# Kernel optimization log

Measured on AMD Instinct MI355X. Metric: run time of the kernel, lower is better.

The kernel has to match this reference:

```python
import jax, jax.numpy as jnp
import numpy as np

N_A, N_B = 100000, 50000
F_IN, C = 32, 64
L, G = 2, 4  # conv layers per gate, gates (i,f,o,c)
E_AA, E_AB, E_BB = 1600000, 800000, 800000


def setup_inputs() -> dict:
    key = jax.random.key(0)
    ks = jax.random.split(key, 15)
    return {
        "x_a": jax.random.normal(ks[0], (N_A, F_IN), jnp.float32),
        "x_b": jax.random.normal(ks[1], (N_B, F_IN), jnp.float32),
        "c_a": jax.random.normal(ks[2], (N_A, C), jnp.float32),
        "c_b": jax.random.normal(ks[3], (N_B, C), jnp.float32),
        "lin_w": jax.random.normal(ks[4], (G, 2, F_IN, C), jnp.float32) * 0.1,
        "lin_b": jax.random.uniform(ks[5], (G, 2, C), jnp.float32),
        "conv_wl": jax.random.normal(ks[6], (G, L, 3, C, C), jnp.float32) * 0.1,
        "conv_wr": jax.random.normal(ks[7], (G, L, 3, C, C), jnp.float32) * 0.1,
        "conv_b": jax.random.uniform(ks[8], (G, L, 3, C), jnp.float32) * 0.1,
        "src_aa": jax.random.randint(ks[9], (E_AA,), 0, N_A),
        "dst_aa": jax.random.randint(ks[10], (E_AA,), 0, N_A),
        "src_ab": jax.random.randint(ks[11], (E_AB,), 0, N_A),
        "dst_ab": jax.random.randint(ks[12], (E_AB,), 0, N_B),
        "src_bb": jax.random.randint(ks[13], (E_BB,), 0, N_B),
        "dst_bb": jax.random.randint(ks[14], (E_BB,), 0, N_B),
    }


def _seg_mean(x_src, src, dst, n_dst):
    # SAGEConv mean aggregation; empty destinations get 0 (PyG semantics)
    s = jax.ops.segment_sum(x_src[src], dst, num_segments=n_dst)
    cnt = jax.ops.segment_sum(jnp.ones((src.shape[0], 1), x_src.dtype), dst, num_segments=n_dst)
    return s / jnp.maximum(cnt, 1.0)


def _gate(g, x_a, x_b, lin_w, lin_b, conv_wl, conv_wr, conv_b, idx):
    src_aa, dst_aa, src_ab, dst_ab, src_bb, dst_bb = idx
    t_a = x_a @ lin_w[g, 0]
    t_b = x_b @ lin_w[g, 1]
    for l in range(L):
        # edge type 0: a->a (dst a)
        agg_aa = _seg_mean(t_a, src_aa, dst_aa, N_A)
        na = agg_aa @ conv_wl[g, l, 0] + t_a @ conv_wr[g, l, 0] + conv_b[g, l, 0]
        # edge types 1: a->b and 2: b->b, HeteroConv sums both into dst b
        agg_ab = _seg_mean(t_a, src_ab, dst_ab, N_B)
        agg_bb = _seg_mean(t_b, src_bb, dst_bb, N_B)
        nb = (agg_ab @ conv_wl[g, l, 1] + t_b @ conv_wr[g, l, 1] + conv_b[g, l, 1]
              + agg_bb @ conv_wl[g, l, 2] + t_b @ conv_wr[g, l, 2] + conv_b[g, l, 2])
        t_a, t_b = na, nb
    return lin_b[g, 0] + t_a, lin_b[g, 1] + t_b


def reference(x_a, x_b, c_a, c_b, lin_w, lin_b, conv_wl, conv_wr, conv_b,
              src_aa, dst_aa, src_ab, dst_ab, src_bb, dst_bb):
    idx = (src_aa, dst_aa, src_ab, dst_ab, src_bb, dst_bb)
    i_a, i_b = map(jax.nn.sigmoid, _gate(0, x_a, x_b, lin_w, lin_b, conv_wl, conv_wr, conv_b, idx))
    f_a, f_b = map(jax.nn.sigmoid, _gate(1, x_a, x_b, lin_w, lin_b, conv_wl, conv_wr, conv_b, idx))
    o_a, o_b = map(jax.nn.sigmoid, _gate(2, x_a, x_b, lin_w, lin_b, conv_wl, conv_wr, conv_b, idx))
    g_a, g_b = map(jnp.tanh, _gate(3, x_a, x_b, lin_w, lin_b, conv_wl, conv_wr, conv_b, idx))
    cn_a = f_a * c_a + i_a * g_a
    cn_b = f_b * c_b + i_b * g_b
    h_a = o_a * jnp.tanh(cn_a)
    h_b = o_b * jnp.tanh(cn_b)
    return (h_a, h_b, cn_a, cn_b)
```

## Files before the change

kernel.cpp:

```cpp
#include <hip/hip_runtime.h>
#include <hip/hip_bf16.h>

#define NA 100000
#define NB 50000
#define EAA 1600000
#define EAB 800000
#define EBB 800000

#define NBKAA 782
#define NBKB  391
#define BKA 200
#define BKB 100
#define DCAP 4096

#define GFA 1563
#define GFB 782

typedef __hip_bfloat16 bf16;
typedef __attribute__((ext_vector_type(8))) short bf16x8;
typedef __attribute__((ext_vector_type(4))) float f32x4;

__device__ __forceinline__ float u2f(unsigned short u) {
  union { unsigned int i; float f; } x; x.i = ((unsigned int)u) << 16; return x.f;
}
__device__ __forceinline__ unsigned short f2u(float f) {
  __hip_bfloat16 h = __float2bfloat16(f);
  return *reinterpret_cast<unsigned short*>(&h);
}
__device__ __forceinline__ short f2bs(float f) {
  __hip_bfloat16 h = __float2bfloat16(f);
  return *reinterpret_cast<short*>(&h);
}
__device__ __forceinline__ float fast_sigmoid(float z) {
  return 1.f / (1.f + __expf(-z));
}
__device__ __forceinline__ float fast_tanh(float z) {
  z = fminf(fmaxf(z, -15.f), 15.f);
  float t = __expf(2.f * z);
  return (t - 1.f) / (t + 1.f);
}

__global__ __launch_bounds__(256) void kA_bin(
    const int* __restrict__ d1, const int* __restrict__ d2, const int* __restrict__ d3,
    int* __restrict__ binAA, int* __restrict__ binAB, int* __restrict__ binBB) {
  __shared__ int h[1024];
  int blk = blockIdx.x;
  const int* dst; int* out; int e0, nbk;
  if (blk < BKA)            { dst = d1; out = binAA + blk * NBKAA; e0 = blk * 8000; nbk = NBKAA; }
  else if (blk < BKA + BKB) { int k = blk - BKA; dst = d2; out = binAB + k * NBKB; e0 = k * 8000; nbk = NBKB; }
  else                      { int k = blk - BKA - BKB; dst = d3; out = binBB + k * NBKB; e0 = k * 8000; nbk = NBKB; }
  for (int i = threadIdx.x; i < nbk; i += 256) h[i] = 0;
  __syncthreads();
  for (int i = threadIdx.x; i < 8000; i += 256) atomicAdd(&h[dst[e0 + i] >> 7], 1);
  __syncthreads();
  for (int i = threadIdx.x; i < nbk; i += 256) out[i] = h[i];
}

__global__ __launch_bounds__(256) void kB1(
    int* __restrict__ binAA, int* __restrict__ binAB, int* __restrict__ binBB,
    int* __restrict__ totAA, int* __restrict__ totAB, int* __restrict__ totBB) {
  int wave = threadIdx.x >> 6, lane = threadIdx.x & 63;
  int wid = blockIdx.x * 4 + wave;
  int* bin; int* tot; int b, nblk, nbk;
  if (wid < NBKAA)              { bin = binAA; tot = totAA; b = wid; nblk = BKA; nbk = NBKAA; }
  else if (wid < NBKAA + NBKB)  { bin = binAB; tot = totAB; b = wid - NBKAA; nblk = BKB; nbk = NBKB; }
  else                          { bin = binBB; tot = totBB; b = wid - NBKAA - NBKB; nblk = BKB; nbk = NBKB; }
  int C = (nblk + 63) / 64;
  int vals[4]; int s = 0;
  for (int j = 0; j < C; ++j) { int k = lane * C + j; vals[j] = (k < nblk) ? bin[k * nbk + b] : 0; s += vals[j]; }
  int pre = s;
  for (int o = 1; o < 64; o <<= 1) { int x = __shfl_up(pre, o); if (lane >= o) pre += x; }
  int run = pre - s;
  for (int j = 0; j < C; ++j) { int k = lane * C + j; if (k < nblk) { int v = vals[j]; bin[k * nbk + b] = run; run += v; } }
  if (lane == 63) tot[b] = pre;
}

__global__ __launch_bounds__(256) void kB2(
    const int* __restrict__ totAA, const int* __restrict__ totAB, const int* __restrict__ totBB,
    int* __restrict__ bsAA, int* __restrict__ bsAB, int* __restrict__ bsBB) {
  __shared__ int part[256];
  int set = blockIdx.x; const int* tot; int* bs; int nbk;
  if (set == 0)      { tot = totAA; bs = bsAA; nbk = NBKAA; }
  else if (set == 1) { tot = totAB; bs = bsAB; nbk = NBKB; }
  else               { tot = totBB; bs = bsBB; nbk = NBKB; }
  int t = threadIdx.x;
  int v[4]; int s = 0;
  #pragma unroll
  for (int j = 0; j < 4; ++j) { int k = t * 4 + j; v[j] = (k < nbk) ? tot[k] : 0; s += v[j]; }
  part[t] = s;
  __syncthreads();
  for (int o = 1; o < 256; o <<= 1) {
    int x = (t >= o) ? part[t - o] : 0;
    __syncthreads();
    part[t] += x;
    __syncthreads();
  }
  int run = part[t] - s;
  #pragma unroll
  for (int j = 0; j < 4; ++j) { int k = t * 4 + j; if (k < nbk) { bs[k] = run; run += v[j]; } }
  if (t == 255) bs[nbk] = part[255];
}

__global__ __launch_bounds__(256) void kC_scatter(
    const int* __restrict__ s1, const int* __restrict__ d1,
    const int* __restrict__ s2, const int* __restrict__ d2,
    const int* __restrict__ s3, const int* __restrict__ d3,
    const int* __restrict__ binAA, const int* __restrict__ binAB, const int* __restrict__ binBB,
    const int* __restrict__ bsAA, const int* __restrict__ bsAB, const int* __restrict__ bsBB,
    int* __restrict__ pkAA, int* __restrict__ pkAB, int* __restrict__ pkBB) {
  __shared__ int baseL[1024];
  __shared__ int run[1024];
  int blk = blockIdx.x;
  const int* src; const int* dst; const int* bin; const int* bs; int* pk; int e0, nbk, bofs;
  if (blk < BKA)            { src = s1; dst = d1; bin = binAA; bs = bsAA; pk = pkAA; e0 = blk * 8000; nbk = NBKAA; bofs = blk * NBKAA; }
  else if (blk < BKA + BKB) { int k = blk - BKA; src = s2; dst = d2; bin = binAB; bs = bsAB; pk = pkAB; e0 = k * 8000; nbk = NBKB; bofs = k * NBKB; }
  else                      { int k = blk - BKA - BKB; src = s3; dst = d3; bin = binBB; bs = bsBB; pk = pkBB; e0 = k * 8000; nbk = NBKB; bofs = k * NBKB; }
  for (int i = threadIdx.x; i < nbk; i += 256) { baseL[i] = bs[i] + bin[bofs + i]; run[i] = 0; }
  __syncthreads();
  for (int i = threadIdx.x; i < 8000; i += 256) {
    int d = dst[e0 + i];
    int b = d >> 7;
    int off = atomicAdd(&run[b], 1);
    pk[baseL[b] + off] = src[e0 + i] | ((d & 127) << 24);
  }
}

__global__ __launch_bounds__(256) void kD_nodesort(
    const int* __restrict__ pkAA, const int* __restrict__ pkAB, const int* __restrict__ pkBB,
    const int* __restrict__ bsAA, const int* __restrict__ bsAB, const int* __restrict__ bsBB,
    int* __restrict__ colAA, int* __restrict__ colAB, int* __restrict__ colBB,
    int* __restrict__ stAA, int* __restrict__ ctAA,
    int* __restrict__ stAB, int* __restrict__ ctAB,
    int* __restrict__ stBB, int* __restrict__ ctBB) {
  __shared__ int hist[128], nodeOff[129], run[128];
  __shared__ int stage[DCAP];
  int wid = blockIdx.x;
  const int* pk; const int* bs; int* col; int* stn; int* ctn; int b, N;
  if (wid < NBKAA)             { pk = pkAA; bs = bsAA; col = colAA; stn = stAA; ctn = ctAA; b = wid; N = NA; }
  else if (wid < NBKAA + NBKB) { pk = pkAB; bs = bsAB; col = colAB; stn = stAB; ctn = ctAB; b = wid - NBKAA; N = NB; }
  else                         { pk = pkBB; bs = bsBB; col = colBB; stn = stBB; ctn = ctBB; b = wid - NBKAA - NBKB; N = NB; }
  int node0 = b * 128;
  int base = bs[b], cntB = bs[b + 1] - base;
  int t = threadIdx.x;
  if (t < 128) hist[t] = 0;
  __syncthreads();
  for (int i = t; i < cntB; i += 256) atomicAdd(&hist[pk[base + i] >> 24], 1);
  __syncthreads();
  if (t < 64) {
    int v0 = hist[2 * t], v1 = hist[2 * t + 1];
    int s = v0 + v1; int pre = s;
    for (int o = 1; o < 64; o <<= 1) { int x = __shfl_up(pre, o); if (t >= o) pre += x; }
    int ex = pre - s;
    nodeOff[2 * t] = ex; nodeOff[2 * t + 1] = ex + v0;
    if (t == 63) nodeOff[128] = pre;
    run[2 * t] = 0; run[2 * t + 1] = 0;
  }
  __syncthreads();
  if (t < 128) {
    int n = node0 + t;
    if (n < N) { ctn[n] = hist[t]; stn[n] = base + nodeOff[t]; }
  }
  if (cntB <= DCAP) {
    for (int i = t; i < cntB; i += 256) {
      int e = pk[base + i]; int ln = e >> 24;
      int off = atomicAdd(&run[ln], 1);
      stage[nodeOff[ln] + off] = e & 0xFFFFFF;
    }
    __syncthreads();
    for (int i = t; i < cntB; i += 256) col[base + i] = stage[i];
  } else {
    for (int i = t; i < cntB; i += 256) {
      int e = pk[base + i]; int ln = e >> 24;
      int off = atomicAdd(&run[ln], 1);
      col[base + nodeOff[ln] + off] = e & 0xFFFFFF;
    }
  }
}

__global__ __launch_bounds__(256) void k_cast2(const float* __restrict__ xa, const float* __restrict__ xb,
                                               bf16* __restrict__ ya, bf16* __restrict__ yb) {
  int i = blockIdx.x * 256 + threadIdx.x;
  const float* x; bf16* y; int base;
  if (i < 800000)       { x = xa; y = ya; base = i * 4; }
  else if (i < 1200000) { x = xb; y = yb; base = (i - 800000) * 4; }
  else return;
  float4 v = *(const float4*)(x + base);
  ushort4 o; o.x = f2u(v.x); o.y = f2u(v.y); o.z = f2u(v.z); o.w = f2u(v.w);
  *(ushort4*)(y + base) = o;
}

__global__ __launch_bounds__(256) void kW1(
    const float* __restrict__ lin_w, const float* __restrict__ wl, const float* __restrict__ wr,
    float* __restrict__ Mbuf) {
  __shared__ float Ls[32][64];
  __shared__ float Rs[64][64];
  int id = blockIdx.x, term = id >> 2, g = id & 3;
  const float* L = lin_w + ((size_t)g * 2 + (term >= 3 ? 1 : 0)) * 2048;
  const float* R1; const float* R2 = nullptr;
  switch (term) {
    case 0: R1 = wl + ((size_t)(g * 2) * 3 + 0) * 4096; break;
    case 1: R1 = wr + ((size_t)(g * 2) * 3 + 0) * 4096; break;
    case 2: R1 = wl + ((size_t)(g * 2) * 3 + 1) * 4096; break;
    case 3: R1 = wl + ((size_t)(g * 2) * 3 + 2) * 4096; break;
    default: R1 = wr + ((size_t)(g * 2) * 3 + 1) * 4096; R2 = wr + ((size_t)(g * 2) * 3 + 2) * 4096; break;
  }
  for (int i = threadIdx.x; i < 2048; i += 256) Ls[i >> 6][i & 63] = L[i];
  for (int i = threadIdx.x; i < 4096; i += 256) Rs[i >> 6][i & 63] = R2 ? (R1[i] + R2[i]) : R1[i];
  __syncthreads();
  int c = threadIdx.x & 63, rq = threadIdx.x >> 6;
  float acc[8] = {0, 0, 0, 0, 0, 0, 0, 0};
  for (int k = 0; k < 64; ++k) {
    float rv = Rs[k][c];
    #pragma unroll
    for (int i = 0; i < 8; ++i) acc[i] += Ls[rq * 8 + i][k] * rv;
  }
  #pragma unroll
  for (int i = 0; i < 8; ++i)
    Mbuf[(size_t)(term * 4 + g) * 2048 + (rq * 8 + i) * 64 + c] = acc[i];
}

__global__ __launch_bounds__(256) void kW2(
    const float* __restrict__ Mbuf, const float* __restrict__ wl, const float* __restrict__ wr,
    const float* __restrict__ cbv, const float* __restrict__ lin_b,
    bf16* __restrict__ Wfrag, float* __restrict__ Bv) {
  __shared__ float Ps[2][32][65];
  __shared__ float Ws[2][64][64];
  int blk = blockIdx.x;
  if (blk >= 36) {
    int g = blk - 36;
    if (threadIdx.x < 64) {
      int c = threadIdx.x;
      const float* b00 = cbv + (size_t)((g * 2 + 0) * 3 + 0) * 64;
      const float* b10 = cbv + (size_t)((g * 2 + 0) * 3 + 1) * 64;
      const float* b20 = cbv + (size_t)((g * 2 + 0) * 3 + 2) * 64;
      const float* b01 = cbv + (size_t)((g * 2 + 1) * 3 + 0) * 64;
      const float* b11 = cbv + (size_t)((g * 2 + 1) * 3 + 1) * 64;
      const float* b21 = cbv + (size_t)((g * 2 + 1) * 3 + 2) * 64;
      const float* wl01 = wl + (size_t)((g * 2 + 1) * 3 + 0) * 4096;
      const float* wl11 = wl + (size_t)((g * 2 + 1) * 3 + 1) * 4096;
      const float* wl21 = wl + (size_t)((g * 2 + 1) * 3 + 2) * 4096;
      const float* wr01 = wr + (size_t)((g * 2 + 1) * 3 + 0) * 4096;
      const float* wr11 = wr + (size_t)((g * 2 + 1) * 3 + 1) * 4096;
      const float* wr21 = wr + (size_t)((g * 2 + 1) * 3 + 2) * 4096;
      float s_maa = 0.f, s_ca = 0.f, s_mab = 0.f, s_mbb = 0.f, s_cb = 0.f;
      for (int k = 0; k < 64; ++k) {
        float v0 = b00[k], vb = b10[k] + b20[k];
        s_maa += v0 * wl01[k * 64 + c];
        s_ca  += v0 * wr01[k * 64 + c];
        s_mab += v0 * wl11[k * 64 + c];
        s_mbb += vb * wl21[k * 64 + c];
        s_cb  += vb * (wr11[k * 64 + c] + wr21[k * 64 + c]);
      }
      Bv[(g * 5 + 0) * 64 + c] = s_maa;
      Bv[(g * 5 + 1) * 64 + c] = s_ca + b01[c] + lin_b[(g * 2 + 0) * 64 + c];
      Bv[(g * 5 + 2) * 64 + c] = s_mab;
      Bv[(g * 5 + 3) * 64 + c] = s_mbb;
      Bv[(g * 5 + 4) * 64 + c] = s_cb + b11[c] + b21[c] + lin_b[(g * 2 + 1) * 64 + c];
    }
    return;
  }
  int mat = blk, g, m;
  if (blk < 12) { g = blk / 3; m = blk % 3; }
  else          { g = (blk - 12) / 6; m = (blk - 12) % 6 + 3; }
  const float* wl01 = wl + (size_t)((g * 2 + 1) * 3 + 0) * 4096;
  const float* wl11 = wl + (size_t)((g * 2 + 1) * 3 + 1) * 4096;
  const float* wl21 = wl + (size_t)((g * 2 + 1) * 3 + 2) * 4096;
  const float* wr01 = wr + (size_t)((g * 2 + 1) * 3 + 0) * 4096;
  const float* wr11 = wr + (size_t)((g * 2 + 1) * 3 + 1) * 4096;
  const float* wr21 = wr + (size_t)((g * 2 + 1) * 3 + 2) * 4096;
  int   p1t, p2t = -1;
  const float *w1a = nullptr, *w1b = nullptr, *w2a = nullptr, *w2b = nullptr;
  switch (m) {
    case 0: p1t = 0; w1a = wl01; break;
    case 1: p1t = 1; w1a = wl01; p2t = 0; w2a = wr01; break;
    case 2: p1t = 1; w1a = wr01; break;
    case 3: p1t = 0; w1a = wl11; break;
    case 4: p1t = 1; w1a = wl11; p2t = 2; w2a = wr11; w2b = wr21; break;
    case 5: p1t = 2; w1a = wl21; break;
    case 6: p1t = 3; w1a = wl21; break;
    case 7: p1t = 3; w1a = wr11; w1b = wr21; p2t = 4; w2a = wl21; break;
    default: p1t = 4; w1a = wr11; w1b = wr21; break;
  }
  int nprod = (p2t >= 0) ? 2 : 1;
  for (int i = threadIdx.x; i < 2048; i += 256) Ps[0][i >> 6][i & 63] = Mbuf[(size_t)(p1t * 4 + g) * 2048 + i];
  for (int i = threadIdx.x; i < 4096; i += 256) Ws[0][i >> 6][i & 63] = w1b ? (w1a[i] + w1b[i]) : w1a[i];
  if (nprod == 2) {
    for (int i = threadIdx.x; i < 2048; i += 256) Ps[1][i >> 6][i & 63] = Mbuf[(size_t)(p2t * 4 + g) * 2048 + i];
    for (int i = threadIdx.x; i < 4096; i += 256) Ws[1][i >> 6][i & 63] = w2b ? (w2a[i] + w2b[i]) : w2a[i];
  }
  __syncthreads();
  int nt = threadIdx.x >> 6, lane = threadIdx.x & 63;
  int c = nt * 16 + (lane & 15), kb = (lane >> 4) * 8;
  float acc[8] = {0, 0, 0, 0, 0, 0, 0, 0};
  for (int k = 0; k < 64; ++k) {
    float w1v = Ws[0][k][c];
    #pragma unroll
    for (int j = 0; j < 8; ++j) acc[j] += Ps[0][kb + j][k] * w1v;
  }
  if (nprod == 2) {
    for (int k = 0; k < 64; ++k) {
      float w2v = Ws[1][k][c];
      #pragma unroll
      for (int j = 0; j < 8; ++j) acc[j] += Ps[1][kb + j][k] * w2v;
    }
  }
  bf16x8 v;
  #pragma unroll
  for (int j = 0; j < 8; ++j) v[j] = f2bs(acc[j]);
  *(bf16x8*)(Wfrag + ((size_t)(mat * 4 + nt) * 64 + lane) * 8) = v;
}

__global__ __launch_bounds__(256) void k_aggP1(
    const bf16* __restrict__ xa, const bf16* __restrict__ xb,
    bf16* __restrict__ P, bf16* __restrict__ Q, bf16* __restrict__ R,
    const int* __restrict__ st_aa, const int* __restrict__ ct_aa, const int* __restrict__ col_aa,
    const int* __restrict__ st_ab, const int* __restrict__ ct_ab, const int* __restrict__ col_ab,
    const int* __restrict__ st_bb, const int* __restrict__ ct_bb, const int* __restrict__ col_bb) {
  int b = blockIdx.x;
  const bf16* src; bf16* dst; const int* start; const int* cnt; const int* col; int n0;
  if (b < 25000)      { src = xa; dst = P; start = st_aa; cnt = ct_aa; col = col_aa; n0 = b * 4; }
  else if (b < 37500) { src = xa; dst = Q; start = st_ab; cnt = ct_ab; col = col_ab; n0 = (b - 25000) * 4; }
  else                { src = xb; dst = R; start = st_bb; cnt = ct_bb; col = col_bb; n0 = (b - 37500) * 4; }
  int wave = threadIdx.x >> 6, lane = threadIdx.x & 63;
  int n = n0 + wave;
  int e8 = lane >> 3, c8 = lane & 7;
  int st = start[n];
  int deg = cnt[n];
  float s0 = 0.f, s1 = 0.f, s2 = 0.f, s3 = 0.f;
  #pragma unroll 2
  for (int e = e8; e < deg; e += 8) {
    int i = col[st + e];
    ushort4 v = *(const ushort4*)(src + (size_t)i * 32 + c8 * 4);
    s0 += u2f(v.x); s1 += u2f(v.y); s2 += u2f(v.z); s3 += u2f(v.w);
  }
  s0 += __shfl_xor(s0, 8);  s1 += __shfl_xor(s1, 8);  s2 += __shfl_xor(s2, 8);  s3 += __shfl_xor(s3, 8);
  s0 += __shfl_xor(s0, 16); s1 += __shfl_xor(s1, 16); s2 += __shfl_xor(s2, 16); s3 += __shfl_xor(s3, 16);
  s0 += __shfl_xor(s0, 32); s1 += __shfl_xor(s1, 32); s2 += __shfl_xor(s2, 32); s3 += __shfl_xor(s3, 32);
  if (e8 == 0) {
    float inv = 1.f / (float)(deg > 1 ? deg : 1);
    ushort4 o; o.x = f2u(s0 * inv); o.y = f2u(s1 * inv); o.z = f2u(s2 * inv); o.w = f2u(s3 * inv);
    *(ushort4*)(dst + (size_t)n * 32 + c8 * 4) = o;
  }
}

__global__ __launch_bounds__(256) void k_aggP2(
    const bf16* __restrict__ P, const bf16* __restrict__ Q, const bf16* __restrict__ R,
    bf16* __restrict__ P2, bf16* __restrict__ Q2, bf16* __restrict__ S, bf16* __restrict__ T,
    const int* __restrict__ st_aa, const int* __restrict__ ct_aa, const int* __restrict__ col_aa,
    const int* __restrict__ st_ab, const int* __restrict__ ct_ab, const int* __restrict__ col_ab,
    const int* __restrict__ st_bb, const int* __restrict__ ct_bb, const int* __restrict__ col_bb) {
  int b = blockIdx.x;
  int wave = threadIdx.x >> 6, lane = threadIdx.x & 63;
  int e8 = lane >> 3, c8 = lane & 7;
  if (b < 37500) {
    const bf16* src; bf16* dst; const int* start; const int* cnt; const int* col; int n0;
    if (b < 25000) { src = P; dst = P2; start = st_aa; cnt = ct_aa; col = col_aa; n0 = b * 4; }
    else           { src = P; dst = Q2; start = st_ab; cnt = ct_ab; col = col_ab; n0 = (b - 25000) * 4; }
    int n = n0 + wave;
    int st = start[n];
    int deg = cnt[n];
    float s0 = 0.f, s1 = 0.f, s2 = 0.f, s3 = 0.f;
    #pragma unroll 2
    for (int e = e8; e < deg; e += 8) {
      int i = col[st + e];
      ushort4 v = *(const ushort4*)(src + (size_t)i * 32 + c8 * 4);
      s0 += u2f(v.x); s1 += u2f(v.y); s2 += u2f(v.z); s3 += u2f(v.w);
    }
    s0 += __shfl_xor(s0, 8);  s1 += __shfl_xor(s1, 8);  s2 += __shfl_xor(s2, 8);  s3 += __shfl_xor(s3, 8);
    s0 += __shfl_xor(s0, 16); s1 += __shfl_xor(s1, 16); s2 += __shfl_xor(s2, 16); s3 += __shfl_xor(s3, 16);
    s0 += __shfl_xor(s0, 32); s1 += __shfl_xor(s1, 32); s2 += __shfl_xor(s2, 32); s3 += __shfl_xor(s3, 32);
    if (e8 == 0) {
      float inv = 1.f / (float)(deg > 1 ? deg : 1);
      ushort4 o; o.x = f2u(s0 * inv); o.y = f2u(s1 * inv); o.z = f2u(s2 * inv); o.w = f2u(s3 * inv);
      *(ushort4*)(dst + (size_t)n * 32 + c8 * 4) = o;
    }
  } else {
    int n = (b - 37500) * 4 + wave;
    int st = st_bb[n];
    int deg = ct_bb[n];
    float q0 = 0.f, q1 = 0.f, q2 = 0.f, q3 = 0.f;
    float r0 = 0.f, r1 = 0.f, r2 = 0.f, r3 = 0.f;
    for (int e = e8; e < deg; e += 8) {
      int i = col_bb[st + e];
      ushort4 vq = *(const ushort4*)(Q + (size_t)i * 32 + c8 * 4);
      ushort4 vr = *(const ushort4*)(R + (size_t)i * 32 + c8 * 4);
      q0 += u2f(vq.x); q1 += u2f(vq.y); q2 += u2f(vq.z); q3 += u2f(vq.w);
      r0 += u2f(vr.x); r1 += u2f(vr.y); r2 += u2f(vr.z); r3 += u2f(vr.w);
    }
    q0 += __shfl_xor(q0, 8);  q1 += __shfl_xor(q1, 8);  q2 += __shfl_xor(q2, 8);  q3 += __shfl_xor(q3, 8);
    r0 += __shfl_xor(r0, 8);  r1 += __shfl_xor(r1, 8);  r2 += __shfl_xor(r2, 8);  r3 += __shfl_xor(r3, 8);
    q0 += __shfl_xor(q0, 16); q1 += __shfl_xor(q1, 16); q2 += __shfl_xor(q2, 16); q3 += __shfl_xor(q3, 16);
    r0 += __shfl_xor(r0, 16); r1 += __shfl_xor(r1, 16); r2 += __shfl_xor(r2, 16); r3 += __shfl_xor(r3, 16);
    q0 += __shfl_xor(q0, 32); q1 += __shfl_xor(q1, 32); q2 += __shfl_xor(q2, 32); q3 += __shfl_xor(q3, 32);
    r0 += __shfl_xor(r0, 32); r1 += __shfl_xor(r1, 32); r2 += __shfl_xor(r2, 32); r3 += __shfl_xor(r3, 32);
    if (e8 == 0) {
      float inv = 1.f / (float)(deg > 1 ? deg : 1);
      ushort4 o1v; o1v.x = f2u(q0 * inv); o1v.y = f2u(q1 * inv); o1v.z = f2u(q2 * inv); o1v.w = f2u(q3 * inv);
      *(ushort4*)(S + (size_t)n * 32 + c8 * 4) = o1v;
      ushort4 o2v; o2v.x = f2u(r0 * inv); o2v.y = f2u(r1 * inv); o2v.z = f2u(r2 * inv); o2v.w = f2u(r3 * inv);
      *(ushort4*)(T + (size_t)n * 32 + c8 * 4) = o2v;
    }
  }
}

__global__ __launch_bounds__(256, 2) void k_fin(
    const bf16* __restrict__ xa, const bf16* __restrict__ P, const bf16* __restrict__ P2,
    const bf16* __restrict__ xb, const bf16* __restrict__ Q, const bf16* __restrict__ R,
    const bf16* __restrict__ Q2, const bf16* __restrict__ S, const bf16* __restrict__ T,
    const bf16* __restrict__ Wfrag, const float* __restrict__ Bv,
    const int* __restrict__ cnt_aa, const int* __restrict__ cnt_ab, const int* __restrict__ cnt_bb,
    const float* __restrict__ c_a, const float* __restrict__ c_b,
    float* __restrict__ out) {
  int blk = blockIdx.x;
  int wave = threadIdx.x >> 6, lane = threadIdx.x & 63;
  int l15 = lane & 15, l4 = lane >> 4;
  const size_t TOTA = (size_t)NA * 64, TOTB = (size_t)NB * 64;
  #define FRAG(mat, nt) (*(const bf16x8*)(Wfrag + ((size_t)((mat) * 4 + (nt)) * 64 + lane) * 8))

  if (blk < GFA) {
    int row0 = (blk * 4 + wave) * 16;
    int r = row0 + l15;
    bool ok = r < NA;
    bf16x8 a0 = {0,0,0,0,0,0,0,0}, a1 = a0, a2 = a0;
    if (ok) {
      a0 = *(const bf16x8*)(P2 + (size_t)r * 32 + l4 * 8);
      a1 = *(const bf16x8*)(P  + (size_t)r * 32 + l4 * 8);
      a2 = *(const bf16x8*)(xa + (size_t)r * 32 + l4 * 8);
    }
    f32x4 z[4][4];
    #pragma unroll
    for (int g = 0; g < 4; ++g) {
      #pragma unroll
      for (int nt = 0; nt < 4; ++nt) {
        f32x4 acc = {0.f, 0.f, 0.f, 0.f};
        acc = __builtin_amdgcn_mfma_f32_16x16x32_bf16(a0, FRAG(g * 3 + 0, nt), acc, 0, 0, 0);
        acc = __builtin_amdgcn_mfma_f32_16x16x32_bf16(a1, FRAG(g * 3 + 1, nt), acc, 0, 0, 0);
        acc = __builtin_amdgcn_mfma_f32_16x16x32_bf16(a2, FRAG(g * 3 + 2, nt), acc, 0, 0, 0);
        z[g][nt] = acc;
      }
    }
    float m[4];
    #pragma unroll
    for (int q = 0; q < 4; ++q) {
      int rr = row0 + l4 * 4 + q;
      m[q] = (rr < NA && cnt_aa[rr] > 0) ? 1.f : 0.f;
    }
    float* h = out;
    float* cn = out + TOTA + TOTB;
    #pragma unroll
    for (int nt = 0; nt < 4; ++nt) {
      int col = nt * 16 + l15;
      #pragma unroll
      for (int q = 0; q < 4; ++q) {
        int rr = row0 + l4 * 4 + q;
        if (rr >= NA) continue;
        float zi = z[0][nt][q] + m[q] * Bv[(0 * 5 + 0) * 64 + col] + Bv[(0 * 5 + 1) * 64 + col];
        float zf = z[1][nt][q] + m[q] * Bv[(1 * 5 + 0) * 64 + col] + Bv[(1 * 5 + 1) * 64 + col];
        float zo = z[2][nt][q] + m[q] * Bv[(2 * 5 + 0) * 64 + col] + Bv[(2 * 5 + 1) * 64 + col];
        float zg = z[3][nt][q] + m[q] * Bv[(3 * 5 + 0) * 64 + col] + Bv[(3 * 5 + 1) * 64 + col];
        float ig = fast_sigmoid(zi);
        float fg = fast_sigmoid(zf);
        float og = fast_sigmoid(zo);
        float gg = fast_tanh(zg);
        size_t idx = (size_t)rr * 64 + col;
        float cv = fg * c_a[idx] + ig * gg;
        h[idx] = og * fast_tanh(cv);
        cn[idx] = cv;
      }
    }
  } else {
    int bb = blk - GFA;
    int row0 = (bb * 4 + wave) * 16;
    int r = row0 + l15;
    bool ok = r < NB;
    bf16x8 a0 = {0,0,0,0,0,0,0,0}, a1 = a0, a2 = a0, a3 = a0, a4 = a0, a5 = a0;
    if (ok) {
      a0 = *(const bf16x8*)(Q2 + (size_t)r * 32 + l4 * 8);
      a1 = *(const bf16x8*)(Q  + (size_t)r * 32 + l4 * 8);
      a2 = *(const bf16x8*)(S  + (size_t)r * 32 + l4 * 8);
      a3 = *(const bf16x8*)(T  + (size_t)r * 32 + l4 * 8);
      a4 = *(const bf16x8*)(R  + (size_t)r * 32 + l4 * 8);
      a5 = *(const bf16x8*)(xb + (size_t)r * 32 + l4 * 8);
    }
    f32x4 z[4][4];
    #pragma unroll
    for (int g = 0; g < 4; ++g) {
      #pragma unroll
      for (int nt = 0; nt < 4; ++nt) {
        int mb = 12 + g * 6;
        f32x4 acc = {0.f, 0.f, 0.f, 0.f};
        acc = __builtin_amdgcn_mfma_f32_16x16x32_bf16(a0, FRAG(mb + 0, nt), acc, 0, 0, 0);
        acc = __builtin_amdgcn_mfma_f32_16x16x32_bf16(a1, FRAG(mb + 1, nt), acc, 0, 0, 0);
        acc = __builtin_amdgcn_mfma_f32_16x16x32_bf16(a2, FRAG(mb + 2, nt), acc, 0, 0, 0);
        acc = __builtin_amdgcn_mfma_f32_16x16x32_bf16(a3, FRAG(mb + 3, nt), acc, 0, 0, 0);
        acc = __builtin_amdgcn_mfma_f32_16x16x32_bf16(a4, FRAG(mb + 4, nt), acc, 0, 0, 0);
        acc = __builtin_amdgcn_mfma_f32_16x16x32_bf16(a5, FRAG(mb + 5, nt), acc, 0, 0, 0);
        z[g][nt] = acc;
      }
    }
    float mab[4], mbb[4];
    #pragma unroll
    for (int q = 0; q < 4; ++q) {
      int rr = row0 + l4 * 4 + q;
      bool okr = rr < NB;
      mab[q] = (okr && cnt_ab[rr] > 0) ? 1.f : 0.f;
      mbb[q] = (okr && cnt_bb[rr] > 0) ? 1.f : 0.f;
    }
    float* h = out + TOTA;
    float* cn = out + 2 * TOTA + TOTB;
    #pragma unroll
    for (int nt = 0; nt < 4; ++nt) {
      int col = nt * 16 + l15;
      #pragma unroll
      for (int q = 0; q < 4; ++q) {
        int rr = row0 + l4 * 4 + q;
        if (rr >= NB) continue;
        float zi = z[0][nt][q] + mab[q] * Bv[(0 * 5 + 2) * 64 + col] + mbb[q] * Bv[(0 * 5 + 3) * 64 + col] + Bv[(0 * 5 + 4) * 64 + col];
        float zf = z[1][nt][q] + mab[q] * Bv[(1 * 5 + 2) * 64 + col] + mbb[q] * Bv[(1 * 5 + 3) * 64 + col] + Bv[(1 * 5 + 4) * 64 + col];
        float zo = z[2][nt][q] + mab[q] * Bv[(2 * 5 + 2) * 64 + col] + mbb[q] * Bv[(2 * 5 + 3) * 64 + col] + Bv[(2 * 5 + 4) * 64 + col];
        float zg = z[3][nt][q] + mab[q] * Bv[(3 * 5 + 2) * 64 + col] + mbb[q] * Bv[(3 * 5 + 3) * 64 + col] + Bv[(3 * 5 + 4) * 64 + col];
        float ig = fast_sigmoid(zi);
        float fg = fast_sigmoid(zf);
        float og = fast_sigmoid(zo);
        float gg = fast_tanh(zg);
        size_t idx = (size_t)rr * 64 + col;
        float cv = fg * c_b[idx] + ig * gg;
        h[idx] = og * fast_tanh(cv);
        cn[idx] = cv;
      }
    }
  }
  #undef FRAG
}

extern "C" void kernel_launch(void* const* d_in, const int* in_sizes, int n_in,
                              void* d_out, int out_size, void* d_ws, size_t ws_size,
                              hipStream_t stream) {
  (void)in_sizes; (void)n_in; (void)out_size; (void)ws_size;
  const float* x_a    = (const float*)d_in[0];
  const float* x_b    = (const float*)d_in[1];
  const float* c_a    = (const float*)d_in[2];
  const float* c_b    = (const float*)d_in[3];
  const float* lin_w  = (const float*)d_in[4];
  const float* lin_b  = (const float*)d_in[5];
  const float* conv_wl = (const float*)d_in[6];
  const float* conv_wr = (const float*)d_in[7];
  const float* conv_cb = (const float*)d_in[8];
  const int* src_aa = (const int*)d_in[9];
  const int* dst_aa = (const int*)d_in[10];
  const int* src_ab = (const int*)d_in[11];
  const int* dst_ab = (const int*)d_in[12];
  const int* src_bb = (const int*)d_in[13];
  const int* dst_bb = (const int*)d_in[14];

  char* ws = (char*)d_ws;
  size_t off = 0;
  auto alloc = [&](size_t bytes) -> char* {
    off = (off + 255) & ~(size_t)255;
    char* p = ws + off;
    off += bytes;
    return p;
  };
  bf16* xab = (bf16*)alloc((size_t)NA * 32 * 2);
  bf16* xbb = (bf16*)alloc((size_t)NB * 32 * 2);
  bf16* P   = (bf16*)alloc((size_t)NA * 32 * 2);
  bf16* P2  = (bf16*)alloc((size_t)NA * 32 * 2);
  bf16* Q   = (bf16*)alloc((size_t)NB * 32 * 2);
  bf16* R   = (bf16*)alloc((size_t)NB * 32 * 2);
  bf16* Q2  = (bf16*)alloc((size_t)NB * 32 * 2);
  bf16* S   = (bf16*)alloc((size_t)NB * 32 * 2);
  bf16* T   = (bf16*)alloc((size_t)NB * 32 * 2);
  float* Mbuf = (float*)alloc((size_t)20 * 2048 * 4);
  bf16* Wfrag = (bf16*)alloc((size_t)36 * 4 * 64 * 8 * 2);
  float* Bv = (float*)alloc((size_t)4 * 5 * 64 * 4);
  int* col_aa  = (int*)alloc((size_t)EAA * 4);
  int* col_ab  = (int*)alloc((size_t)EAB * 4);
  int* col_bb  = (int*)alloc((size_t)EBB * 4);
  int* pk_aa   = (int*)alloc((size_t)EAA * 4);
  int* pk_ab   = (int*)alloc((size_t)EAB * 4);
  int* pk_bb   = (int*)alloc((size_t)EBB * 4);
  int* start_aa = (int*)alloc((size_t)NA * 4);
  int* start_ab = (int*)alloc((size_t)NB * 4);
  int* start_bb = (int*)alloc((size_t)NB * 4);
  int* cnt_aa  = (int*)alloc((size_t)NA * 4);
  int* cnt_ab  = (int*)alloc((size_t)NB * 4);
  int* cnt_bb  = (int*)alloc((size_t)NB * 4);
  int* binAA   = (int*)alloc((size_t)BKA * NBKAA * 4);
  int* binAB   = (int*)alloc((size_t)BKB * NBKB * 4);
  int* binBB   = (int*)alloc((size_t)BKB * NBKB * 4);
  int* totAA   = (int*)alloc((size_t)NBKAA * 4);
  int* totAB   = (int*)alloc((size_t)NBKB * 4);
  int* totBB   = (int*)alloc((size_t)NBKB * 4);
  int* bsAA    = (int*)alloc((size_t)(NBKAA + 1) * 4);
  int* bsAB    = (int*)alloc((size_t)(NBKB + 1) * 4);
  int* bsBB    = (int*)alloc((size_t)(NBKB + 1) * 4);

  kW1<<<20, 256, 0, stream>>>(lin_w, conv_wl, conv_wr, Mbuf);
  kW2<<<40, 256, 0, stream>>>(Mbuf, conv_wl, conv_wr, conv_cb, lin_b, Wfrag, Bv);
  k_cast2<<<4688, 256, 0, stream>>>(x_a, x_b, xab, xbb);

  kA_bin<<<BKA + 2 * BKB, 256, 0, stream>>>(dst_aa, dst_ab, dst_bb, binAA, binAB, binBB);
  kB1<<<(NBKAA + 2 * NBKB) / 4, 256, 0, stream>>>(binAA, binAB, binBB, totAA, totAB, totBB);
  kB2<<<3, 256, 0, stream>>>(totAA, totAB, totBB, bsAA, bsAB, bsBB);
  kC_scatter<<<BKA + 2 * BKB, 256, 0, stream>>>(src_aa, dst_aa, src_ab, dst_ab, src_bb, dst_bb,
                                                binAA, binAB, binBB, bsAA, bsAB, bsBB,
                                                pk_aa, pk_ab, pk_bb);
  kD_nodesort<<<NBKAA + 2 * NBKB, 256, 0, stream>>>(pk_aa, pk_ab, pk_bb, bsAA, bsAB, bsBB,
                                                    col_aa, col_ab, col_bb,
                                                    start_aa, cnt_aa, start_ab, cnt_ab,
                                                    start_bb, cnt_bb);

  k_aggP1<<<50000, 256, 0, stream>>>(xab, xbb, P, Q, R,
                                     start_aa, cnt_aa, col_aa,
                                     start_ab, cnt_ab, col_ab,
                                     start_bb, cnt_bb, col_bb);
  k_aggP2<<<50000, 256, 0, stream>>>(P, Q, R, P2, Q2, S, T,
                                     start_aa, cnt_aa, col_aa,
                                     start_ab, cnt_ab, col_ab,
                                     start_bb, cnt_bb, col_bb);

  k_fin<<<GFA + GFB, 256, 0, stream>>>(xab, P, P2, xbb, Q, R, Q2, S, T,
                                       Wfrag, Bv, cnt_aa, cnt_ab, cnt_bb,
                                       c_a, c_b, (float*)d_out);
}
```

Before: 304.2 us.

## Shrink edge blocks, widen gather loads, and process 32 rows per wave in k_fin

Result: slower. 334.3 us (+9.9%).

```diff
diff --git a/kernel.cpp b/kernel.cpp
--- a/kernel.cpp
+++ b/kernel.cpp
@@ -9,12 +9,13 @@
 
 #define NBKAA 782
 #define NBKB  391
-#define BKA 200
-#define BKB 100
+#define EPB 2000
+#define BKA 800
+#define BKB 400
 #define DCAP 4096
 
-#define GFA 1563
-#define GFB 782
+#define GF2A 782
+#define GF2B 391
 
 typedef __hip_bfloat16 bf16;
 typedef __attribute__((ext_vector_type(8))) short bf16x8;
@@ -46,12 +47,12 @@
   __shared__ int h[1024];
   int blk = blockIdx.x;
   const int* dst; int* out; int e0, nbk;
-  if (blk < BKA)            { dst = d1; out = binAA + blk * NBKAA; e0 = blk * 8000; nbk = NBKAA; }
-  else if (blk < BKA + BKB) { int k = blk - BKA; dst = d2; out = binAB + k * NBKB; e0 = k * 8000; nbk = NBKB; }
-  else                      { int k = blk - BKA - BKB; dst = d3; out = binBB + k * NBKB; e0 = k * 8000; nbk = NBKB; }
+  if (blk < BKA)            { dst = d1; out = binAA + blk * NBKAA; e0 = blk * EPB; nbk = NBKAA; }
+  else if (blk < BKA + BKB) { int k = blk - BKA; dst = d2; out = binAB + k * NBKB; e0 = k * EPB; nbk = NBKB; }
+  else                      { int k = blk - BKA - BKB; dst = d3; out = binBB + k * NBKB; e0 = k * EPB; nbk = NBKB; }
   for (int i = threadIdx.x; i < nbk; i += 256) h[i] = 0;
   __syncthreads();
-  for (int i = threadIdx.x; i < 8000; i += 256) atomicAdd(&h[dst[e0 + i] >> 7], 1);
+  for (int i = threadIdx.x; i < EPB; i += 256) atomicAdd(&h[dst[e0 + i] >> 7], 1);
   __syncthreads();
   for (int i = threadIdx.x; i < nbk; i += 256) out[i] = h[i];
 }
@@ -66,7 +67,7 @@
   else if (wid < NBKAA + NBKB)  { bin = binAB; tot = totAB; b = wid - NBKAA; nblk = BKB; nbk = NBKB; }
   else                          { bin = binBB; tot = totBB; b = wid - NBKAA - NBKB; nblk = BKB; nbk = NBKB; }
   int C = (nblk + 63) / 64;
-  int vals[4]; int s = 0;
+  int vals[16]; int s = 0;
   for (int j = 0; j < C; ++j) { int k = lane * C + j; vals[j] = (k < nblk) ? bin[k * nbk + b] : 0; s += vals[j]; }
   int pre = s;
   for (int o = 1; o < 64; o <<= 1) { int x = __shfl_up(pre, o); if (lane >= o) pre += x; }
@@ -112,12 +113,12 @@
   __shared__ int run[1024];
   int blk = blockIdx.x;
   const int* src; const int* dst; const int* bin; const int* bs; int* pk; int e0, nbk, bofs;
-  if (blk < BKA)            { src = s1; dst = d1; bin = binAA; bs = bsAA; pk = pkAA; e0 = blk * 8000; nbk = NBKAA; bofs = blk * NBKAA; }
-  else if (blk < BKA + BKB) { int k = blk - BKA; src = s2; dst = d2; bin = binAB; bs = bsAB; pk = pkAB; e0 = k * 8000; nbk = NBKB; bofs = k * NBKB; }
-  else                      { int k = blk - BKA - BKB; src = s3; dst = d3; bin = binBB; bs = bsBB; pk = pkBB; e0 = k * 8000; nbk = NBKB; bofs = k * NBKB; }
+  if (blk < BKA)            { src = s1; dst = d1; bin = binAA; bs = bsAA; pk = pkAA; e0 = blk * EPB; nbk = NBKAA; bofs = blk * NBKAA; }
+  else if (blk < BKA + BKB) { int k = blk - BKA; src = s2; dst = d2; bin = binAB; bs = bsAB; pk = pkAB; e0 = k * EPB; nbk = NBKB; bofs = k * NBKB; }
+  else                      { int k = blk - BKA - BKB; src = s3; dst = d3; bin = binBB; bs = bsBB; pk = pkBB; e0 = k * EPB; nbk = NBKB; bofs = k * NBKB; }
   for (int i = threadIdx.x; i < nbk; i += 256) { baseL[i] = bs[i] + bin[bofs + i]; run[i] = 0; }
   __syncthreads();
-  for (int i = threadIdx.x; i < 8000; i += 256) {
+  for (int i = threadIdx.x; i < EPB; i += 256) {
     int d = dst[e0 + i];
     int b = d >> 7;
     int off = atomicAdd(&run[b], 1);
@@ -310,6 +311,30 @@
   *(bf16x8*)(Wfrag + ((size_t)(mat * 4 + nt) * 64 + lane) * 8) = v;
 }
 
+__device__ __forceinline__ void acc8(float* s, uint4 v) {
+  s[0] += u2f((unsigned short)(v.x & 0xFFFF)); s[1] += u2f((unsigned short)(v.x >> 16));
+  s[2] += u2f((unsigned short)(v.y & 0xFFFF)); s[3] += u2f((unsigned short)(v.y >> 16));
+  s[4] += u2f((unsigned short)(v.z & 0xFFFF)); s[5] += u2f((unsigned short)(v.z >> 16));
+  s[6] += u2f((unsigned short)(v.w & 0xFFFF)); s[7] += u2f((unsigned short)(v.w >> 16));
+}
+__device__ __forceinline__ void red16(float* s) {
+  #pragma unroll
+  for (int j = 0; j < 8; ++j) {
+    s[j] += __shfl_xor(s[j], 4);
+    s[j] += __shfl_xor(s[j], 8);
+    s[j] += __shfl_xor(s[j], 16);
+    s[j] += __shfl_xor(s[j], 32);
+  }
+}
+__device__ __forceinline__ uint4 pack8(const float* s, float inv) {
+  uint4 o;
+  o.x = (unsigned)f2u(s[0] * inv) | ((unsigned)f2u(s[1] * inv) << 16);
+  o.y = (unsigned)f2u(s[2] * inv) | ((unsigned)f2u(s[3] * inv) << 16);
+  o.z = (unsigned)f2u(s[4] * inv) | ((unsigned)f2u(s[5] * inv) << 16);
+  o.w = (unsigned)f2u(s[6] * inv) | ((unsigned)f2u(s[7] * inv) << 16);
+  return o;
+}
+
 __global__ __launch_bounds__(256) void k_aggP1(
     const bf16* __restrict__ xa, const bf16* __restrict__ xb,
     bf16* __restrict__ P, bf16* __restrict__ Q, bf16* __restrict__ R,
@@ -323,23 +348,19 @@
   else                { src = xb; dst = R; start = st_bb; cnt = ct_bb; col = col_bb; n0 = (b - 37500) * 4; }
   int wave = threadIdx.x >> 6, lane = threadIdx.x & 63;
   int n = n0 + wave;
-  int e8 = lane >> 3, c8 = lane & 7;
+  int e16 = lane >> 2, c4 = lane & 3;
   int st = start[n];
   int deg = cnt[n];
-  float s0 = 0.f, s1 = 0.f, s2 = 0.f, s3 = 0.f;
-  #pragma unroll 2
-  for (int e = e8; e < deg; e += 8) {
+  float s[8] = {0, 0, 0, 0, 0, 0, 0, 0};
+  for (int e = e16; e < deg; e += 16) {
     int i = col[st + e];
-    ushort4 v = *(const ushort4*)(src + (size_t)i * 32 + c8 * 4);
-    s0 += u2f(v.x); s1 += u2f(v.y); s2 += u2f(v.z); s3 += u2f(v.w);
-  }
-  s0 += __shfl_xor(s0, 8);  s1 += __shfl_xor(s1, 8);  s2 += __shfl_xor(s2, 8);  s3 += __shfl_xor(s3, 8);
-  s0 += __shfl_xor(s0, 16); s1 += __shfl_xor(s1, 16); s2 += __shfl_xor(s2, 16); s3 += __shfl_xor(s3, 16);
-  s0 += __shfl_xor(s0, 32); s1 += __shfl_xor(s1, 32); s2 += __shfl_xor(s2, 32); s3 += __shfl_xor(s3, 32);
-  if (e8 == 0) {
+    uint4 v = *(const uint4*)(src + (size_t)i * 32 + c4 * 8);
+    acc8(s, v);
+  }
+  red16(s);
+  if (e16 == 0) {
     float inv = 1.f / (float)(deg > 1 ? deg : 1);
-    ushort4 o; o.x = f2u(s0 * inv); o.y = f2u(s1 * inv); o.z = f2u(s2 * inv); o.w = f2u(s3 * inv);
-    *(ushort4*)(dst + (size_t)n * 32 + c8 * 4) = o;
+    *(uint4*)(dst + (size_t)n * 32 + c4 * 8) = pack8(s, inv);
   }
 }
 
@@ -351,7 +372,7 @@
     const int* __restrict__ st_bb, const int* __restrict__ ct_bb, const int* __restrict__ col_bb) {
   int b = blockIdx.x;
   int wave = threadIdx.x >> 6, lane = threadIdx.x & 63;
-  int e8 = lane >> 3, c8 = lane & 7;
+  int e16 = lane >> 2, c4 = lane & 3;
   if (b < 37500) {
     const bf16* src; bf16* dst; const int* start; const int* cnt; const int* col; int n0;
     if (b < 25000) { src = P; dst = P2; start = st_aa; cnt = ct_aa; col = col_aa; n0 = b * 4; }
@@ -359,51 +380,41 @@
     int n = n0 + wave;
     int st = start[n];
     int deg = cnt[n];
-    float s0 = 0.f, s1 = 0.f, s2 = 0.f, s3 = 0.f;
-    #pragma unroll 2
-    for (int e = e8; e < deg; e += 8) {
+    float s[8] = {0, 0, 0, 0, 0, 0, 0, 0};
+    for (int e = e16; e < deg; e += 16) {
       int i = col[st + e];
-      ushort4 v = *(const ushort4*)(src + (size_t)i * 32 + c8 * 4);
-      s0 += u2f(v.x); s1 += u2f(v.y); s2 += u2f(v.z); s3 += u2f(v.w);
-    }
-    s0 += __shfl_xor(s0, 8);  s1 += __shfl_xor(s1, 8);  s2 += __shfl_xor(s2, 8);  s3 += __shfl_xor(s3, 8);
-    s0 += __shfl_xor(s0, 16); s1 += __shfl_xor(s1, 16); s2 += __shfl_xor(s2, 16); s3 += __shfl_xor(s3, 16);
-    s0 += __shfl_xor(s0, 32); s1 += __shfl_xor(s1, 32); s2 += __shfl_xor(s2, 32); s3 += __shfl_xor(s3, 32);
-    if (e8 == 0) {
+      uint4 v = *(const uint4*)(src + (size_t)i * 32 + c4 * 8);
+      acc8(s, v);
+    }
+    red16(s);
+    if (e16 == 0) {
       float inv = 1.f / (float)(deg > 1 ? deg : 1);
-      ushort4 o; o.x = f2u(s0 * inv); o.y = f2u(s1 * inv); o.z = f2u(s2 * inv); o.w = f2u(s3 * inv);
-      *(ushort4*)(dst + (size_t)n * 32 + c8 * 4) = o;
+      *(uint4*)(dst + (size_t)n * 32 + c4 * 8) = pack8(s, inv);
     }
   } else {
     int n = (b - 37500) * 4 + wave;
     int st = st_bb[n];
     int deg = ct_bb[n];
-    float q0 = 0.f, q1 = 0.f, q2 = 0.f, q3 = 0.f;
-    float r0 = 0.f, r1 = 0.f, r2 = 0.f, r3 = 0.f;
-    for (int e = e8; e < deg; e += 8) {
+    float sq[8] = {0, 0, 0, 0, 0, 0, 0, 0};
+    float sr[8] = {0, 0, 0, 0, 0, 0, 0, 0};
+    for (int e = e16; e < deg; e += 16) {
       int i = col_bb[st + e];
-      ushort4 vq = *(const ushort4*)(Q + (size_t)i * 32 + c8 * 4);
-      ushort4 vr = *(const ushort4*)(R + (size_t)i * 32 + c8 * 4);
-      q0 += u2f(vq.x); q1 += u2f(vq.y); q2 += u2f(vq.z); q3 += u2f(vq.w);
-      r0 += u2f(vr.x); r1 += u2f(vr.y); r2 += u2f(vr.z); r3 += u2f(vr.w);
-    }
-    q0 += __shfl_xor(q0, 8);  q1 += __shfl_xor(q1, 8);  q2 += __shfl_xor(q2, 8);  q3 += __shfl_xor(q3, 8);
-    r0 += __shfl_xor(r0, 8);  r1 += __shfl_xor(r1, 8);  r2 += __shfl_xor(r2, 8);  r3 += __shfl_xor(r3, 8);
-    q0 += __shfl_xor(q0, 16); q1 += __shfl_xor(q1, 16); q2 += __shfl_xor(q2, 16); q3 += __shfl_xor(q3, 16);
-    r0 += __shfl_xor(r0, 16); r1 += __shfl_xor(r1, 16); r2 += __shfl_xor(r2, 16); r3 += __shfl_xor(r3, 16);
-    q0 += __shfl_xor(q0, 32); q1 += __shfl_xor(q1, 32); q2 += __shfl_xor(q2, 32); q3 += __shfl_xor(q3, 32);
-    r0 += __shfl_xor(r0, 32); r1 += __shfl_xor(r1, 32); r2 += __shfl_xor(r2, 32); r3 += __shfl_xor(r3, 32);
-    if (e8 == 0) {
+      uint4 vq = *(const uint4*)(Q + (size_t)i * 32 + c4 * 8);
+      uint4 vr = *(const uint4*)(R + (size_t)i * 32 + c4 * 8);
+      acc8(sq, vq);
+      acc8(sr, vr);
+    }
+    red16(sq);
+    red16(sr);
+    if (e16 == 0) {
       float inv = 1.f / (float)(deg > 1 ? deg : 1);
-      ushort4 o1v; o1v.x = f2u(q0 * inv); o1v.y = f2u(q1 * inv); o1v.z = f2u(q2 * inv); o1v.w = f2u(q3 * inv);
-      *(ushort4*)(S + (size_t)n * 32 + c8 * 4) = o1v;
-      ushort4 o2v; o2v.x = f2u(r0 * inv); o2v.y = f2u(r1 * inv); o2v.z = f2u(r2 * inv); o2v.w = f2u(r3 * inv);
-      *(ushort4*)(T + (size_t)n * 32 + c8 * 4) = o2v;
-    }
-  }
-}
-
-__global__ __launch_bounds__(256, 2) void k_fin(
+      *(uint4*)(S + (size_t)n * 32 + c4 * 8) = pack8(sq, inv);
+      *(uint4*)(T + (size_t)n * 32 + c4 * 8) = pack8(sr, inv);
+    }
+  }
+}
+
+__global__ __launch_bounds__(256) void k_fin(
     const bf16* __restrict__ xa, const bf16* __restrict__ P, const bf16* __restrict__ P2,
     const bf16* __restrict__ xb, const bf16* __restrict__ Q, const bf16* __restrict__ R,
     const bf16* __restrict__ Q2, const bf16* __restrict__ S, const bf16* __restrict__ T,
@@ -416,117 +427,151 @@
   int l15 = lane & 15, l4 = lane >> 4;
   const size_t TOTA = (size_t)NA * 64, TOTB = (size_t)NB * 64;
   #define FRAG(mat, nt) (*(const bf16x8*)(Wfrag + ((size_t)((mat) * 4 + (nt)) * 64 + lane) * 8))
-
-  if (blk < GFA) {
-    int row0 = (blk * 4 + wave) * 16;
-    int r = row0 + l15;
-    bool ok = r < NA;
-    bf16x8 a0 = {0,0,0,0,0,0,0,0}, a1 = a0, a2 = a0;
-    if (ok) {
-      a0 = *(const bf16x8*)(P2 + (size_t)r * 32 + l4 * 8);
-      a1 = *(const bf16x8*)(P  + (size_t)r * 32 + l4 * 8);
-      a2 = *(const bf16x8*)(xa + (size_t)r * 32 + l4 * 8);
-    }
-    f32x4 z[4][4];
+  const bf16x8 z8 = {0, 0, 0, 0, 0, 0, 0, 0};
+
+  if (blk < GF2A) {
+    int row0 = (blk * 4 + wave) * 32;
+    bf16x8 a[3][2];
+    float m[2][4];
     #pragma unroll
-    for (int g = 0; g < 4; ++g) {
-      #pragma unroll
-      for (int nt = 0; nt < 4; ++nt) {
-        f32x4 acc = {0.f, 0.f, 0.f, 0.f};
-        acc = __builtin_amdgcn_mfma_f32_16x16x32_bf16(a0, FRAG(g * 3 + 0, nt), acc, 0, 0, 0);
-        acc = __builtin_amdgcn_mfma_f32_16x16x32_bf16(a1, FRAG(g * 3 + 1, nt), acc, 0, 0, 0);
-        acc = __builtin_amdgcn_mfma_f32_16x16x32_bf16(a2, FRAG(g * 3 + 2, nt), acc, 0, 0, 0);
-        z[g][nt] = acc;
+    for (int s = 0; s < 2; ++s) {
+      int r = row0 + s * 16 + l15;
+      bool ok = r < NA;
+      a[0][s] = ok ? *(const bf16x8*)(P2 + (size_t)r * 32 + l4 * 8) : z8;
+      a[1][s] = ok ? *(const bf16x8*)(P  + (size_t)r * 32 + l4 * 8) : z8;
+      a[2][s] = ok ? *(const bf16x8*)(xa + (size_t)r * 32 + l4 * 8) : z8;
+      #pragma unroll
+      for (int q = 0; q < 4; ++q) {
+        int rr = row0 + s * 16 + l4 * 4 + q;
+        m[s][q] = (rr < NA && cnt_aa[rr] > 0) ? 1.f : 0.f;
       }
-    }
-    float m[4];
-    #pragma unroll
-    for (int q = 0; q < 4; ++q) {
-      int rr = row0 + l4 * 4 + q;
-      m[q] = (rr < NA && cnt_aa[rr] > 0) ? 1.f : 0.f;
     }
     float* h = out;
     float* cn = out + TOTA + TOTB;
     #pragma unroll
     for (int nt = 0; nt < 4; ++nt) {
       int col = nt * 16 + l15;
+      bf16x8 fr[12];
+      #pragma unroll
+      for (int gq = 0; gq < 12; ++gq) fr[gq] = FRAG(gq, nt);
+      float bm[4], bc[4];
+      #pragma unroll
+      for (int g = 0; g < 4; ++g) { bm[g] = Bv[(g * 5 + 0) * 64 + col]; bc[g] = Bv[(g * 5 + 1) * 64 + col]; }
+      #pragma unroll
+      for (int s = 0; s < 2; ++s) {
+        float cpre[4];
+        #pragma unroll
+        for (int q = 0; q < 4; ++q) {
+          int rr = row0 + s * 16 + l4 * 4 + q;
+          cpre[q] = (rr < NA) ? c_a[(size_t)rr * 64 + col] : 0.f;
+        }
+        f32x4 z[4];
+        #pragma unroll
+        for (int g = 0; g < 4; ++g) {
+          f32x4 acc = {0.f, 0.f, 0.f, 0.f};
+          acc = __builtin_amdgcn_mfma_f32_16x16x32_bf16(a[0][s], fr[g * 3 + 0], acc, 0, 0, 0);
+          acc = __builtin_amdgcn_mfma_f32_16x16x32_bf16(a[1][s], fr[g * 3 + 1], acc, 0, 0, 0);
+          acc = __builtin_amdgcn_mfma_f32_16x16x32_bf16(a[2][s], fr[g * 3 + 2], acc, 0, 0, 0);
+          z[g] = acc;
+        }
+        #pragma unroll
+        for (int q = 0; q < 4; ++q) {
+          int rr = row0 + s * 16 + l4 * 4 + q;
+          if (rr >= NA) continue;
+          float zi = z[0][q] + m[s][q] * bm[0] + bc[0];
+          float zf = z[1][q] + m[s][q] * bm[1] + bc[1];
+          float zo = z[2][q] + m[s][q] * bm[2] + bc[2];
+          float zg = z[3][q] + m[s][q] * bm[3] + bc[3];
+          float ig = fast_sigmoid(zi);
+          float fg = fast_sigmoid(zf);
+          float og = fast_sigmoid(zo);
+          float gg = fast_tanh(zg);
+          size_t idx = (size_t)rr * 64 + col;
+          float cv = fg * cpre[q] + ig * gg;
+          h[idx] = og * fast_tanh(cv);
+          cn[idx] = cv;
+        }
+      }
+    }
+  } else {
+    int bb = blk - GF2A;
+    int row0 = (bb * 4 + wave) * 32;
+    bf16x8 a[6][2];
+    float mab[2][4], mbb[2][4];
+    #pragma unroll
+    for (int s = 0; s < 2; ++s) {
+      int r = row0 + s * 16 + l15;
+      bool ok = r < NB;
+      a[0][s] = ok ? *(const bf16x8*)(Q2 + (size_t)r * 32 + l4 * 8) : z8;
+      a[1][s] = ok ? *(const bf16x8*)(Q  + (size_t)r * 32 + l4 * 8) : z8;
+      a[2][s] = ok ? *(const bf16x8*)(S  + (size_t)r * 32 + l4 * 8) : z8;
+      a[3][s] = ok ? *(const bf16x8*)(T  + (size_t)r * 32 + l4 * 8) : z8;
+      a[4][s] = ok ? *(const bf16x8*)(R  + (size_t)r * 32 + l4 * 8) : z8;
+      a[5][s] = ok ? *(const bf16x8*)(xb + (size_t)r * 32 + l4 * 8) : z8;
       #pragma unroll
       for (int q = 0; q < 4; ++q) {
-        int rr = row0 + l4 * 4 + q;
-        if (rr >= NA) continue;
-        float zi = z[0][nt][q] + m[q] * Bv[(0 * 5 + 0) * 64 + col] + Bv[(0 * 5 + 1) * 64 + col];
-        float zf = z[1][nt][q] + m[q] * Bv[(1 * 5 + 0) * 64 + col] + Bv[(1 * 5 + 1) * 64 + col];
-        float zo = z[2][nt][q] + m[q] * Bv[(2 * 5 + 0) * 64 + col] + Bv[(2 * 5 + 1) * 64 + col];
-        float zg = z[3][nt][q] + m[q] * Bv[(3 * 5 + 0) * 64 + col] + Bv[(3 * 5 + 1) * 64 + col];
-        float ig = fast_sigmoid(zi);
-        float fg = fast_sigmoid(zf);
-        float og = fast_sigmoid(zo);
-        float gg = fast_tanh(zg);
-        size_t idx = (size_t)rr * 64 + col;
-        float cv = fg * c_a[idx] + ig * gg;
-        h[idx] = og * fast_tanh(cv);
-        cn[idx] = cv;
+        int rr = row0 + s * 16 + l4 * 4 + q;
+        bool okr = rr < NB;
+        mab[s][q] = (okr && cnt_ab[rr] > 0) ? 1.f : 0.f;
+        mbb[s][q] = (okr && cnt_bb[rr] > 0) ? 1.f : 0.f;
       }
-    }
-  } else {
-    int bb = blk - GFA;
-    int row0 = (bb * 4 + wave) * 16;
-    int r = row0 + l15;
-    bool ok = r < NB;
-    bf16x8 a0 = {0,0,0,0,0,0,0,0}, a1 = a0, a2 = a0, a3 = a0, a4 = a0, a5 = a0;
-    if (ok) {
-      a0 = *(const bf16x8*)(Q2 + (size_t)r * 32 + l4 * 8);
-      a1 = *(const bf16x8*)(Q  + (size_t)r * 32 + l4 * 8);
-      a2 = *(const bf16x8*)(S  + (size_t)r * 32 + l4 * 8);
-      a3 = *(const bf16x8*)(T  + (size_t)r * 32 + l4 * 8);
-      a4 = *(const bf16x8*)(R  + (size_t)r * 32 + l4 * 8);
-      a5 = *(const bf16x8*)(xb + (size_t)r * 32 + l4 * 8);
-    }
-    f32x4 z[4][4];
-    #pragma unroll
-    for (int g = 0; g < 4; ++g) {
-      #pragma unroll
-      for (int nt = 0; nt < 4; ++nt) {
-        int mb = 12 + g * 6;
-        f32x4 acc = {0.f, 0.f, 0.f, 0.f};
-        acc = __builtin_amdgcn_mfma_f32_16x16x32_bf16(a0, FRAG(mb + 0, nt), acc, 0, 0, 0);
-        acc = __builtin_amdgcn_mfma_f32_16x16x32_bf16(a1, FRAG(mb + 1, nt), acc, 0, 0, 0);
-        acc = __builtin_amdgcn_mfma_f32_16x16x32_bf16(a2, FRAG(mb + 2, nt), acc, 0, 0, 0);
-        acc = __builtin_amdgcn_mfma_f32_16x16x32_bf16(a3, FRAG(mb + 3, nt), acc, 0, 0, 0);
-        acc = __builtin_amdgcn_mfma_f32_16x16x32_bf16(a4, FRAG(mb + 4, nt), acc, 0, 0, 0);
-        acc = __builtin_amdgcn_mfma_f32_16x16x32_bf16(a5, FRAG(mb + 5, nt), acc, 0, 0, 0);
-        z[g][nt] = acc;
-      }
-    }
-    float mab[4], mbb[4];
-    #pragma unroll
-    for (int q = 0; q < 4; ++q) {
-      int rr = row0 + l4 * 4 + q;
-      bool okr = rr < NB;
-      mab[q] = (okr && cnt_ab[rr] > 0) ? 1.f : 0.f;
-      mbb[q] = (okr && cnt_bb[rr] > 0) ? 1.f : 0.f;
     }
     float* h = out + TOTA;
     float* cn = out + 2 * TOTA + TOTB;
     #pragma unroll
     for (int nt = 0; nt < 4; ++nt) {
       int col = nt * 16 + l15;
-      #pragma unroll
-      for (int q = 0; q < 4; ++q) {
-        int rr = row0 + l4 * 4 + q;
-        if (rr >= NB) continue;
-        float zi = z[0][nt][q] + mab[q] * Bv[(0 * 5 + 2) * 64 + col] + mbb[q] * Bv[(0 * 5 + 3) * 64 + col] + Bv[(0 * 5 + 4) * 64 + col];
-        float zf = z[1][nt][q] + mab[q] * Bv[(1 * 5 + 2) * 64 + col] + mbb[q] * Bv[(1 * 5 + 3) * 64 + col] + Bv[(1 * 5 + 4) * 64 + col];
-        float zo = z[2][nt][q] + mab[q] * Bv[(2 * 5 + 2) * 64 + col] + mbb[q] * Bv[(2 * 5 + 3) * 64 + col] + Bv[(2 * 5 + 4) * 64 + col];
-        float zg = z[3][nt][q] + mab[q] * Bv[(3 * 5 + 2) * 64 + col] + mbb[q] * Bv[(3 * 5 + 3) * 64 + col] + Bv[(3 * 5 + 4) * 64 + col];
-        float ig = fast_sigmoid(zi);
-        float fg = fast_sigmoid(zf);
-        float og = fast_sigmoid(zo);
-        float gg = fast_tanh(zg);
-        size_t idx = (size_t)rr * 64 + col;
-        float cv = fg * c_b[idx] + ig * gg;
-        h[idx] = og * fast_tanh(cv);
-        cn[idx] = cv;
+      float bm1[4], bm2[4], bc[4];
+      #pragma unroll
+      for (int g = 0; g < 4; ++g) {
+        bm1[g] = Bv[(g * 5 + 2) * 64 + col];
+        bm2[g] = Bv[(g * 5 + 3) * 64 + col];
+        bc[g]  = Bv[(g * 5 + 4) * 64 + col];
+      }
+      float cpre[2][4];
+      #pragma unroll
+      for (int s = 0; s < 2; ++s)
+        #pragma unroll
+        for (int q = 0; q < 4; ++q) {
+          int rr = row0 + s * 16 + l4 * 4 + q;
+          cpre[s][q] = (rr < NB) ? c_b[(size_t)rr * 64 + col] : 0.f;
+        }
+      f32x4 z[2][4];
+      #pragma unroll
+      for (int s = 0; s < 2; ++s)
+        #pragma unroll
+        for (int g = 0; g < 4; ++g) z[s][g] = (f32x4){0.f, 0.f, 0.f, 0.f};
+      #pragma unroll
+      for (int g = 0; g < 4; ++g) {
+        bf16x8 fr[6];
+        #pragma unroll
+        for (int t = 0; t < 6; ++t) fr[t] = FRAG(12 + g * 6 + t, nt);
+        #pragma unroll
+        for (int s = 0; s < 2; ++s) {
+          #pragma unroll
+          for (int t = 0; t < 6; ++t)
+            z[s][g] = __builtin_amdgcn_mfma_f32_16x16x32_bf16(a[t][s], fr[t], z[s][g], 0, 0, 0);
+        }
+      }
+      #pragma unroll
+      for (int s = 0; s < 2; ++s) {
+        #pragma unroll
+        for (int q = 0; q < 4; ++q) {
+          int rr = row0 + s * 16 + l4 * 4 + q;
+          if (rr >= NB) continue;
+          float zi = z[s][0][q] + mab[s][q] * bm1[0] + mbb[s][q] * bm2[0] + bc[0];
+          float zf = z[s][1][q] + mab[s][q] * bm1[1] + mbb[s][q] * bm2[1] + bc[1];
+          float zo = z[s][2][q] + mab[s][q] * bm1[2] + mbb[s][q] * bm2[2] + bc[2];
+          float zg = z[s][3][q] + mab[s][q] * bm1[3] + mbb[s][q] * bm2[3] + bc[3];
+          float ig = fast_sigmoid(zi);
+          float fg = fast_sigmoid(zf);
+          float og = fast_sigmoid(zo);
+          float gg = fast_tanh(zg);
+          size_t idx = (size_t)rr * 64 + col;
+          float cv = fg * cpre[s][q] + ig * gg;
+          h[idx] = og * fast_tanh(cv);
+          cn[idx] = cv;
+        }
       }
     }
   }
@@ -619,7 +664,7 @@
                                      start_ab, cnt_ab, col_ab,
                                      start_bb, cnt_bb, col_bb);
 
-  k_fin<<<GFA + GFB, 256, 0, stream>>>(xab, P, P2, xbb, Q, R, Q2, S, T,
-                                       Wfrag, Bv, cnt_aa, cnt_ab, cnt_bb,
-                                       c_a, c_b, (float*)d_out);
-}
+  k_fin<<<GF2A + GF2B, 256, 0, stream>>>(xab, P, P2, xbb, Q, R, Q2, S, T,
+                                         Wfrag, Bv, cnt_aa, cnt_ab, cnt_bb,
+                                         c_a, c_b, (float*)d_out);
+}
```
